# Kernel tuning notes

Hardware: AMD Instinct MI355X
Metric: run time of the kernel (lower is better)

Reference implementation:

```python
import jax, jax.numpy as jnp
import numpy as np

DIM = 4096
N_HEADS = 32
N_KV_HEADS = 8
HEAD_DIM = 128
N_REP = N_HEADS // N_KV_HEADS  # 4
Q_DIM = N_HEADS * HEAD_DIM     # 4096
K_DIM = N_KV_HEADS * HEAD_DIM  # 1024
B, T = 2, 2048
ROPE_THETA = 10000.0


def setup_inputs() -> dict:
    key = jax.random.key(0)
    k1, k2, k3, k4 = jax.random.split(key, 4)
    x = jax.random.normal(k1, (B, T, DIM), dtype=jnp.float32)
    wqkv = jax.random.normal(k2, (Q_DIM + 2 * K_DIM, DIM), dtype=jnp.float32) * 0.02
    wo = jax.random.normal(k3, (DIM, DIM), dtype=jnp.float32) * 0.02
    # RoPE tables: [max_T, head_dim//2]
    inv_freq = 1.0 / (ROPE_THETA ** (jnp.arange(0, HEAD_DIM, 2, dtype=jnp.float32) / HEAD_DIM))
    angles = jnp.arange(T, dtype=jnp.float32)[:, None] * inv_freq[None, :]  # [T, D/2]
    cos = jnp.cos(angles)
    sin = jnp.sin(angles)
    freqs_cis = jax.random.normal(k4, (T, HEAD_DIM // 2), dtype=jnp.float32)  # unused by forward
    return {"x": x, "freqs_cis": freqs_cis, "wqkv": wqkv, "wo": wo, "cos": cos, "sin": sin}


def _apply_rope(q, k, cos, sin):
    # q: [B,T,Hq,D], k: [B,T,Hkv,D]; interleaved even/odd pairs
    Tlen = q.shape[1]
    c = cos[:Tlen][None, :, None, :]  # [1,T,1,D/2]
    s = sin[:Tlen][None, :, None, :]

    def rot(t):
        tr, ti = t[..., 0::2], t[..., 1::2]
        or_ = tr * c - ti * s
        oi = tr * s + ti * c
        return jnp.stack([or_, oi], axis=-1).reshape(t.shape)

    return rot(q), rot(k)


def reference(x, freqs_cis, wqkv, wo, cos, sin):
    Bx, Tx, _ = x.shape
    qkv = jnp.einsum('btd,ed->bte', x, wqkv)  # fused QKV GEMM
    q = qkv[..., :Q_DIM].reshape(Bx, Tx, N_HEADS, HEAD_DIM)
    k = qkv[..., Q_DIM:Q_DIM + K_DIM].reshape(Bx, Tx, N_KV_HEADS, HEAD_DIM)
    v = qkv[..., Q_DIM + K_DIM:].reshape(Bx, Tx, N_KV_HEADS, HEAD_DIM)
    q, k = _apply_rope(q, k, cos, sin)
    # GQA repeat_interleave over head dim
    k = jnp.repeat(k, N_REP, axis=2)  # [B,T,Hq,D]
    v = jnp.repeat(v, N_REP, axis=2)
    scale = 1.0 / jnp.sqrt(jnp.asarray(HEAD_DIM, dtype=q.dtype))
    scores = jnp.einsum('bqhd,bkhd->bhqk', q, k) * scale  # [B,H,T,T]
    causal = jnp.tril(jnp.ones((Tx, Tx), dtype=bool))
    scores = jnp.where(causal[None, None], scores, jnp.finfo(scores.dtype).min)
    probs = jax.nn.softmax(scores, axis=-1)
    y = jnp.einsum('bhqk,bkhd->bqhd', probs, v).reshape(Bx, Tx, Q_DIM)
    return jnp.einsum('btd,ed->bte', y, wo)
```

## Files before the change

kernel.cpp:

```cpp
#include <hip/hip_runtime.h>

#define T_SEQ 2048
#define NB    2
#define NH    32
#define NKV   8
#define HD    128
#define DIM   4096
#define EDIM  6144
#define M_TOK 4096

typedef __bf16          bf8  __attribute__((ext_vector_type(8)));
typedef unsigned short  us8  __attribute__((ext_vector_type(8)));
typedef float           f4   __attribute__((ext_vector_type(4)));
typedef float           f16v __attribute__((ext_vector_type(16)));
typedef int             i4   __attribute__((ext_vector_type(4)));

__device__ inline unsigned short f2bf(float f) {
  unsigned int u = __builtin_bit_cast(unsigned int, f);
  u += 0x7FFF + ((u >> 16) & 1);
  return (unsigned short)(u >> 16);
}
__device__ inline float bf2f(unsigned short h) {
  unsigned int u = ((unsigned int)h) << 16;
  return __builtin_bit_cast(float, u);
}
__device__ inline void gl_lds16(const void* g, void* l) {
  __builtin_amdgcn_global_load_lds(
      (const __attribute__((address_space(1))) unsigned int*)g,
      (__attribute__((address_space(3))) unsigned int*)l, 16, 0, 0);
}
__device__ inline f4 mfma16(bf8 a, bf8 b, f4 c) {
  return __builtin_amdgcn_mfma_f32_16x16x32_bf16(a, b, c, 0, 0, 0);
}
__device__ inline f16v mfma32(bf8 a, bf8 b, f16v c) {
  return __builtin_amdgcn_mfma_f32_32x32x16_bf16(a, b, c, 0, 0, 0);
}
__device__ inline unsigned cvtpk(float lo, float hi) {
  unsigned r;
  asm("v_cvt_pk_bf16_f32 %0, %1, %2" : "=v"(r) : "v"(lo), "v"(hi));
  return r;
}

__global__ void k_f2bf3(const float* __restrict__ x, const float* __restrict__ wq,
                        const float* __restrict__ wo,
                        unsigned short* __restrict__ xb, unsigned short* __restrict__ wqb,
                        unsigned short* __restrict__ wob) {
  const long n0 = (long)M_TOK * DIM / 4;
  const long n1 = (long)EDIM * DIM / 4;
  const long n2 = (long)DIM * DIM / 4;
  const long total = n0 + n1 + n2;
  const long stride = (long)gridDim.x * blockDim.x;
  for (long i = (long)blockIdx.x * blockDim.x + threadIdx.x; i < total; i += stride) {
    const float* in; unsigned short* out; long j = i;
    if (j < n0)              { in = x;  out = xb; }
    else if ((j -= n0) < n1) { in = wq; out = wqb; }
    else       { j -= n1;      in = wo; out = wob; }
    f4 v = *(const f4*)(in + j * 4);
    unsigned long long pack =
        (unsigned long long)f2bf(v[0]) |
        ((unsigned long long)f2bf(v[1]) << 16) |
        ((unsigned long long)f2bf(v[2]) << 32) |
        ((unsigned long long)f2bf(v[3]) << 48);
    *(unsigned long long*)(out + j * 4) = pack;
  }
}

__global__ __launch_bounds__(512, 2)
void k_gemm384(const unsigned short* __restrict__ A, const unsigned short* __restrict__ Bm,
               unsigned short* __restrict__ oQ, unsigned short* __restrict__ oK,
               unsigned short* __restrict__ oV) {
  __shared__ unsigned short As[2][8192];
  __shared__ unsigned short Bs[2][3][8192];
  const int n0 = blockIdx.x;
  const int x = n0 & 7, ix = n0 >> 3;
  const int bm = ((x >> 1) << 3) + (ix >> 3);
  const int bn = ((x & 1) << 3) + (ix & 7);
  const int t = threadIdx.x;
  const int lane = t & 63, w = t >> 6;
  const int wr = w >> 2, wc = w & 3;
  const int l15 = lane & 15, lhi = lane >> 4;
  const int KT = DIM >> 6;

  f4 acc[4][6] = {};

  const int tt0 = t * 8;
  auto stA = [&](int buf, int tile) {
    if (tile >= KT) return;
    const unsigned short* gp = A + (size_t)(bm * 128) * DIM + tile * 64;
#pragma unroll
    for (int j = 0; j < 2; ++j) {
      int e = j * 4096 + tt0;
      int rl = e >> 6, cs = (e & 63) ^ ((rl & 7) << 3);
      gl_lds16(gp + (size_t)rl * DIM + cs, &As[buf][e]);
    }
  };
  auto stB = [&](int buf, int bh, int tile) {
    if (tile >= KT) return;
    const unsigned short* gp = Bm + (size_t)(bn * 384 + bh * 128) * DIM + tile * 64;
#pragma unroll
    for (int j = 0; j < 2; ++j) {
      int e = j * 4096 + tt0;
      int rl = e >> 6, cs = (e & 63) ^ ((rl & 7) << 3);
      gl_lds16(gp + (size_t)rl * DIM + cs, &Bs[buf][bh][e]);
    }
  };
  auto rdA = [&](int buf, int mi, int kk) -> bf8 {
    int row = wr * 64 + mi * 16 + l15;
    int col = (lhi * 8 + kk * 32) ^ ((row & 7) << 3);
    return __builtin_bit_cast(bf8, *(const us8*)&As[buf][row * 64 + col]);
  };
  auto rdB = [&](int buf, int bh, int ni, int kk) -> bf8 {
    int row = wc * 32 + ni * 16 + l15;
    int col = (lhi * 8 + kk * 32) ^ ((row & 7) << 3);
    return __builtin_bit_cast(bf8, *(const us8*)&Bs[buf][bh][row * 64 + col]);
  };
  auto bar = [&]() {
    asm volatile("" ::: "memory");
    __builtin_amdgcn_s_barrier();
    asm volatile("" ::: "memory");
  };
  auto lgkm0 = [&]() {
    asm volatile("s_waitcnt lgkmcnt(0)" ::: "memory");
    __builtin_amdgcn_sched_barrier(0);
  };

  stA(0, 0); stB(0, 0, 0); stB(0, 1, 0); stB(0, 2, 0);
  asm volatile("s_waitcnt vmcnt(4)" ::: "memory");
  bar();

  for (int tp = 0; tp < KT; tp += 2) {
#pragma unroll
    for (int sub = 0; sub < 2; ++sub) {
      const int tc = tp + sub, b = sub;
      const bool last = (tc == KT - 1);
      bf8 af[4][2], bfr[2][2];
#pragma unroll
      for (int mi = 0; mi < 4; ++mi)
#pragma unroll
        for (int kk = 0; kk < 2; ++kk) af[mi][kk] = rdA(b, mi, kk);
#pragma unroll
      for (int ni = 0; ni < 2; ++ni)
#pragma unroll
        for (int kk = 0; kk < 2; ++kk) bfr[ni][kk] = rdB(b, 0, ni, kk);
      stA(b ^ 1, tc + 1); stB(b ^ 1, 0, tc + 1);
      lgkm0();
      __builtin_amdgcn_s_setprio(1);
#pragma unroll
      for (int mi = 0; mi < 4; ++mi)
#pragma unroll
        for (int ni = 0; ni < 2; ++ni)
#pragma unroll
          for (int kk = 0; kk < 2; ++kk)
            acc[mi][ni] = mfma16(af[mi][kk], bfr[ni][kk], acc[mi][ni]);
      __builtin_amdgcn_s_setprio(0);
      if (last) { asm volatile("s_waitcnt vmcnt(2)" ::: "memory"); }
      else      { asm volatile("s_waitcnt vmcnt(6)" ::: "memory"); }
      bar();
#pragma unroll
      for (int ni = 0; ni < 2; ++ni)
#pragma unroll
        for (int kk = 0; kk < 2; ++kk) bfr[ni][kk] = rdB(b, 1, ni, kk);
      stB(b ^ 1, 1, tc + 1);
      lgkm0();
      __builtin_amdgcn_s_setprio(1);
#pragma unroll
      for (int mi = 0; mi < 4; ++mi)
#pragma unroll
        for (int ni = 0; ni < 2; ++ni)
#pragma unroll
          for (int kk = 0; kk < 2; ++kk)
            acc[mi][2 + ni] = mfma16(af[mi][kk], bfr[ni][kk], acc[mi][2 + ni]);
      __builtin_amdgcn_s_setprio(0);
      if (last) { asm volatile("s_waitcnt vmcnt(0)" ::: "memory"); }
      else      { asm volatile("s_waitcnt vmcnt(6)" ::: "memory"); }
      bar();
#pragma unroll
      for (int ni = 0; ni < 2; ++ni)
#pragma unroll
        for (int kk = 0; kk < 2; ++kk) bfr[ni][kk] = rdB(b, 2, ni, kk);
      stB(b ^ 1, 2, tc + 1);
      lgkm0();
      __builtin_amdgcn_s_setprio(1);
#pragma unroll
      for (int mi = 0; mi < 4; ++mi)
#pragma unroll
        for (int ni = 0; ni < 2; ++ni)
#pragma unroll
          for (int kk = 0; kk < 2; ++kk)
            acc[mi][4 + ni] = mfma16(af[mi][kk], bfr[ni][kk], acc[mi][4 + ni]);
      __builtin_amdgcn_s_setprio(0);
      if (!last) { asm volatile("s_waitcnt vmcnt(4)" ::: "memory"); }
      bar();
    }
  }

#pragma unroll
  for (int bh = 0; bh < 3; ++bh)
#pragma unroll
    for (int ni = 0; ni < 2; ++ni) {
      const int colb = bn * 384 + bh * 128 + wc * 32 + ni * 16;
      unsigned short* op; int ldo, c0;
      if (colb < 4096)      { op = oQ; ldo = 4096; c0 = colb; }
      else if (colb < 5120) { op = oK; ldo = 1024; c0 = colb - 4096; }
      else                  { op = oV; ldo = 1024; c0 = colb - 5120; }
#pragma unroll
      for (int mi = 0; mi < 4; ++mi)
#pragma unroll
        for (int rr = 0; rr < 4; ++rr) {
          int row = bm * 128 + wr * 64 + mi * 16 + lhi * 4 + rr;
          op[(size_t)row * ldo + c0 + l15] = f2bf(acc[mi][bh * 2 + ni][rr]);
        }
    }
}

#define MFMA_Q(a0, b0, AF, BF)                                        \
  __builtin_amdgcn_s_setprio(1);                                      \
  _Pragma("unroll") for (int mi = 0; mi < 4; ++mi)                    \
  _Pragma("unroll") for (int ni = 0; ni < 2; ++ni)                    \
  _Pragma("unroll") for (int kk = 0; kk < 2; ++kk)                    \
      acc[(a0) + mi][(b0) + ni] =                                     \
          mfma16(AF[mi][kk], BF[ni][kk], acc[(a0) + mi][(b0) + ni]);  \
  __builtin_amdgcn_s_setprio(0);

#define RD_A(buf, mh)                                                 \
  _Pragma("unroll") for (int mi = 0; mi < 4; ++mi)                    \
  _Pragma("unroll") for (int kk = 0; kk < 2; ++kk)                    \
      af[mi][kk] = rdA(buf, mh, mi, kk);

#define RD_B(buf, nh, BF)                                             \
  _Pragma("unroll") for (int ni = 0; ni < 2; ++ni)                    \
  _Pragma("unroll") for (int kk = 0; kk < 2; ++kk)                    \
      BF[ni][kk] = rdB(buf, nh, ni, kk);

__global__ __launch_bounds__(512, 2)
void k_gemm256f(const unsigned short* __restrict__ A, const unsigned short* __restrict__ Bm,
                float* __restrict__ oF) {
  __shared__ unsigned short As[2][16384];
  __shared__ unsigned short Bs[2][16384];
  const int n0 = blockIdx.x;
  const int x = n0 & 7, ix = n0 >> 3;
  const int bm = ((x >> 1) << 2) + (ix >> 3);
  const int bn = ((x & 1) << 3) + (ix & 7);
  const int N = DIM, K = DIM;
  const int t = threadIdx.x;
  const int lane = t & 63, w = t >> 6;
  const int wr = w >> 2, wc = w & 3;
  const int l15 = lane & 15, lhi = lane >> 4;
  const int KT = K >> 6;
  const int NI = KT >> 1;

  f4 acc[8][4] = {};

  const int tt0 = t * 8;
  auto stA = [&](int buf, int half, int tile) {
    if (tile >= KT) return;
    const unsigned short* gp = A + (size_t)(bm * 256 + half * 128) * K + tile * 64;
#pragma unroll
    for (int j = 0; j < 2; ++j) {
      int e = j * 4096 + tt0;
      int rl = e >> 6;
      int cs = (e & 63) ^ ((rl & 7) << 3);
      gl_lds16(gp + (size_t)rl * K + cs, &As[buf][half * 8192 + e]);
    }
  };
  auto stB = [&](int buf, int half, int tile) {
    if (tile >= KT) return;
    const unsigned short* gp = Bm + (size_t)(bn * 256 + half * 128) * K + tile * 64;
#pragma unroll
    for (int j = 0; j < 2; ++j) {
      int e = j * 4096 + tt0;
      int rl = e >> 6;
      int cs = (e & 63) ^ ((rl & 7) << 3);
      gl_lds16(gp + (size_t)rl * K + cs, &Bs[buf][half * 8192 + e]);
    }
  };
  auto rdA = [&](int buf, int mh, int mi, int kk) -> bf8 {
    int row = mh * 128 + wr * 64 + mi * 16 + l15;
    int col = (lhi * 8 + kk * 32) ^ ((row & 7) << 3);
    return __builtin_bit_cast(bf8, *(const us8*)&As[buf][row * 64 + col]);
  };
  auto rdB = [&](int buf, int nh, int ni, int kk) -> bf8 {
    int row = nh * 128 + wc * 32 + ni * 16 + l15;
    int col = (lhi * 8 + kk * 32) ^ ((row & 7) << 3);
    return __builtin_bit_cast(bf8, *(const us8*)&Bs[buf][row * 64 + col]);
  };
  auto bar = [&]() {
    asm volatile("" ::: "memory");
    __builtin_amdgcn_s_barrier();
    asm volatile("" ::: "memory");
  };
  auto lgkm0 = [&]() {
    asm volatile("s_waitcnt lgkmcnt(0)" ::: "memory");
    __builtin_amdgcn_sched_barrier(0);
  };

  stA(0, 0, 0); stB(0, 1, 0); stA(0, 1, 0); stB(0, 0, 0);
  stA(1, 0, 1); stB(1, 1, 1); stA(1, 1, 1);
  asm volatile("s_waitcnt vmcnt(6)" ::: "memory");
  bar();

  for (int i = 0; i < NI; ++i) {
    const int t2 = 2 * i + 2, t3 = 2 * i + 3;
    bf8 af[4][2], bf0[2][2], bf1[2][2];
    RD_A(0, 0); RD_B(0, 0, bf0);
    stB(1, 0, 2 * i + 1);
    lgkm0();
    MFMA_Q(0, 0, af, bf0);
    bar();
    RD_B(0, 1, bf1);
    stA(0, 0, t2);
    lgkm0();
    MFMA_Q(0, 2, af, bf1);
    bar();
    RD_A(0, 1);
    stB(0, 1, t2);
    lgkm0();
    MFMA_Q(4, 2, af, bf1);
    bar();
    stA(0, 1, t2);
    MFMA_Q(4, 0, af, bf0);
    if (i + 1 < NI) { asm volatile("s_waitcnt vmcnt(6)" ::: "memory"); }
    else            { asm volatile("s_waitcnt vmcnt(0)" ::: "memory"); }
    bar();
    RD_A(1, 0); RD_B(1, 0, bf0);
    stB(0, 0, t2);
    lgkm0();
    MFMA_Q(0, 0, af, bf0);
    bar();
    RD_B(1, 1, bf1);
    stA(1, 0, t3);
    lgkm0();
    MFMA_Q(0, 2, af, bf1);
    bar();
    RD_A(1, 1);
    stB(1, 1, t3);
    lgkm0();
    MFMA_Q(4, 2, af, bf1);
    bar();
    stA(1, 1, t3);
    MFMA_Q(4, 0, af, bf0);
    if (i + 1 < NI) { asm volatile("s_waitcnt vmcnt(6)" ::: "memory"); }
    bar();
  }

  const int rb0 = bm * 256 + wr * 64 + lhi * 4;
  const int cb0 = bn * 256 + wc * 32 + l15;
#pragma unroll
  for (int ai = 0; ai < 8; ++ai)
#pragma unroll
    for (int bj = 0; bj < 4; ++bj)
#pragma unroll
      for (int rr = 0; rr < 4; ++rr) {
        int row = rb0 + (ai >> 2) * 128 + (ai & 3) * 16 + rr;
        int col = cb0 + (bj >> 1) * 128 + (bj & 1) * 16;
        oF[(size_t)row * N + col] = acc[ai][bj][rr];
      }
}

__global__ __launch_bounds__(512, 2)
void k_attn(const unsigned short* __restrict__ Qb, const unsigned short* __restrict__ Kb,
            const unsigned short* __restrict__ Vb, unsigned short* __restrict__ Yb,
            const float* __restrict__ cosp, const float* __restrict__ sinp) {
  __shared__ unsigned short Ks[64 * 128];
  __shared__ unsigned short Vt[128 * 64];
  const int idx = blockIdx.x;
  const int qblk = 7 - (idx >> 6);
  const int h = (idx & 63) >> 1;
  const int b = idx & 1;
  const int kvh = h >> 2;
  const int t = threadIdx.x;
  const int lane = t & 63, w = t >> 6;
  const int l31 = lane & 31, hh = lane >> 5;
  const int qb0 = qblk * 256;
  const int NT = (qblk + 1) * 4;
  const int wqmin = qb0 + w * 32;
  const int q_g = wqmin + l31;
  const float BNEG = -1.0e30f;
  const float QSCALE = (float)(0.08838834764831845 * 1.4426950408889634);

  bf8 qf[8];
  {
    const unsigned short* qp = Qb + (size_t)(b * T_SEQ + q_g) * 4096 + h * 128 + hh * 8;
#pragma unroll
    for (int st = 0; st < 8; ++st) {
      us8 v = *(const us8*)(qp + st * 16);
      f4 c = *(const f4*)(cosp + q_g * 64 + st * 8 + hh * 4);
      f4 s = *(const f4*)(sinp + q_g * 64 + st * 8 + hh * 4);
      us8 o;
#pragma unroll
      for (int j = 0; j < 4; ++j) {
        float tr = bf2f(v[2 * j]), ti = bf2f(v[2 * j + 1]);
        o[2 * j]     = f2bf((tr * c[j] - ti * s[j]) * QSCALE);
        o[2 * j + 1] = f2bf((tr * s[j] + ti * c[j]) * QSCALE);
      }
      qf[st] = __builtin_bit_cast(bf8, o);
    }
  }
  const int swz = (l31 & 7) << 3;
  float m_run = BNEG, l_run = 0.f;
  f16v yacc[4] = {};

  const int krow = t >> 4;
  const int kcol = (t & 15) * 8;
  for (int kt = 0; kt < NT; ++kt) {
    const int kbase = kt * 64;
    const unsigned short* vp = Vb + (size_t)(b * T_SEQ + kbase + lane) * 1024 + kvh * 128 + w * 8;
    us8 vv0 = *(const us8*)vp;
    us8 vv1 = *(const us8*)(vp + 64);
    const unsigned short* kp = Kb + (size_t)(b * T_SEQ + kbase + krow) * 1024 + kvh * 128 + kcol;
    us8 kk0 = *(const us8*)kp;
    us8 kk1 = *(const us8*)(kp + (size_t)32 * 1024);
    f4 kc0 = *(const f4*)(cosp + (kbase + krow) * 64 + (kcol >> 1));
    f4 ks0 = *(const f4*)(sinp + (kbase + krow) * 64 + (kcol >> 1));
    f4 kc1 = *(const f4*)(cosp + (kbase + krow + 32) * 64 + (kcol >> 1));
    f4 ks1 = *(const f4*)(sinp + (kbase + krow + 32) * 64 + (kcol >> 1));
    __syncthreads();
    {
      us8 o0, o1;
#pragma unroll
      for (int j = 0; j < 4; ++j) {
        float tr0 = bf2f(kk0[2 * j]), ti0 = bf2f(kk0[2 * j + 1]);
        o0[2 * j]     = f2bf(tr0 * kc0[j] - ti0 * ks0[j]);
        o0[2 * j + 1] = f2bf(tr0 * ks0[j] + ti0 * kc0[j]);
        float tr1 = bf2f(kk1[2 * j]), ti1 = bf2f(kk1[2 * j + 1]);
        o1[2 * j]     = f2bf(tr1 * kc1[j] - ti1 * ks1[j]);
        o1[2 * j + 1] = f2bf(tr1 * ks1[j] + ti1 * kc1[j]);
      }
      *(us8*)&Ks[krow * 128 + (kcol ^ ((krow & 7) << 3))] = o0;
      *(us8*)&Ks[(krow + 32) * 128 + (kcol ^ ((krow & 7) << 3))] = o1;
    }
#pragma unroll
    for (int j = 0; j < 8; ++j) {
      int d0 = w * 8 + j;
      Vt[(d0 * 64 + lane) ^ ((d0 & 7) << 3)] = vv0[j];
      int d1 = d0 + 64;
      Vt[(d1 * 64 + lane) ^ ((d1 & 7) << 3)] = vv1[j];
    }
    __syncthreads();
    if (kbase > wqmin + 31) continue;

    f16v s0 = {}, s1 = {};
#pragma unroll
    for (int st = 0; st < 8; ++st) {
      int coff = st * 16 + hh * 8;
      bf8 a0 = __builtin_bit_cast(bf8, *(const us8*)&Ks[(l31 * 128 + coff) ^ swz]);
      bf8 a1 = __builtin_bit_cast(bf8, *(const us8*)&Ks[((l31 + 32) * 128 + coff) ^ swz]);
      s0 = mfma32(a0, qf[st], s0);
      s1 = mfma32(a1, qf[st], s1);
    }
    if (kbase + 63 > wqmin) {
#pragma unroll
      for (int r = 0; r < 16; ++r) {
        int kv = kbase + (r & 3) + 8 * (r >> 2) + 4 * hh;
        if (kv > q_g)      s0[r] = BNEG;
        if (kv + 32 > q_g) s1[r] = BNEG;
      }
    }
    float tmax = BNEG;
#pragma unroll
    for (int r = 0; r < 16; ++r) {
      tmax = fmaxf(tmax, s0[r]);
      tmax = fmaxf(tmax, s1[r]);
    }
    tmax = fmaxf(tmax, __shfl_xor(tmax, 32));
    float m_new = fmaxf(m_run, tmax);
    float fac = exp2f(m_run - m_new);
    m_run = m_new;
    float psum = 0.f;
#pragma unroll
    for (int r = 0; r < 16; ++r) {
      s0[r] = exp2f(s0[r] - m_new); psum += s0[r];
      s1[r] = exp2f(s1[r] - m_new); psum += s1[r];
    }
    psum += __shfl_xor(psum, 32);
    l_run = l_run * fac + psum;
    if (!__all(fac == 1.0f)) {
      float facr[16];
#pragma unroll
      for (int r = 0; r < 16; ++r)
        facr[r] = __shfl(fac, (r & 3) + 8 * (r >> 2) + 4 * hh);
#pragma unroll
      for (int dc = 0; dc < 4; ++dc)
#pragma unroll
        for (int r = 0; r < 16; ++r) yacc[dc][r] *= facr[r];
    }
#pragma unroll
    for (int st = 0; st < 4; ++st) {
      f16v sv = (st & 2) ? s1 : s0;
      const int rb = (st & 1) * 8;
      unsigned pkA = cvtpk(sv[rb + 0], sv[rb + 1]);
      unsigned pkB = cvtpk(sv[rb + 2], sv[rb + 3]);
      unsigned pkC = cvtpk(sv[rb + 4], sv[rb + 5]);
      unsigned pkD = cvtpk(sv[rb + 6], sv[rb + 7]);
      unsigned xA = __shfl_xor(pkA, 32);
      unsigned xB = __shfl_xor(pkB, 32);
      unsigned xC = __shfl_xor(pkC, 32);
      unsigned xD = __shfl_xor(pkD, 32);
      unsigned w0 = hh ? xC : pkA;
      unsigned w1 = hh ? xD : pkB;
      unsigned w2 = hh ? pkC : xA;
      unsigned w3 = hh ? pkD : xB;
      i4 wi = { (int)w0, (int)w1, (int)w2, (int)w3 };
      bf8 pf = __builtin_bit_cast(bf8, wi);
#pragma unroll
      for (int dc = 0; dc < 4; ++dc) {
        int d = dc * 32 + l31;
        bf8 vf = __builtin_bit_cast(bf8, *(const us8*)&Vt[(d * 64 + st * 16 + hh * 8) ^ swz]);
        yacc[dc] = mfma32(pf, vf, yacc[dc]);
      }
    }
  }
  float inv_l = 1.0f / l_run;
  float il[16];
#pragma unroll
  for (int r = 0; r < 16; ++r)
    il[r] = __shfl(inv_l, (r & 3) + 8 * (r >> 2) + 4 * hh);
#pragma unroll
  for (int dc = 0; dc < 4; ++dc)
#pragma unroll
    for (int r = 0; r < 16; ++r) {
      int qrow = qb0 + w * 32 + (r & 3) + 8 * (r >> 2) + 4 * hh;
      Yb[(size_t)(b * T_SEQ + qrow) * 4096 + h * 128 + dc * 32 + l31] =
          f2bf(yacc[dc][r] * il[r]);
    }
}

extern "C" void kernel_launch(void* const* d_in, const int* in_sizes, int n_in,
                              void* d_out, int out_size, void* d_ws, size_t ws_size,
                              hipStream_t stream) {
  const float* x    = (const float*)d_in[0];
  const float* wqkv = (const float*)d_in[2];
  const float* wo   = (const float*)d_in[3];
  const float* cosp = (const float*)d_in[4];
  const float* sinp = (const float*)d_in[5];
  float* out = (float*)d_out;

  char* ws = (char*)d_ws;
  size_t o = 0;
  auto alloc = [&](size_t bytes) { void* p = ws + o; o += (bytes + 255) & ~(size_t)255; return p; };
  unsigned short* x_b    = (unsigned short*)alloc((size_t)M_TOK * DIM * 2);
  unsigned short* wqkv_b = (unsigned short*)alloc((size_t)EDIM * DIM * 2);
  unsigned short* wo_b   = (unsigned short*)alloc((size_t)DIM * DIM * 2);
  unsigned short* Qb     = (unsigned short*)alloc((size_t)M_TOK * 4096 * 2);
  unsigned short* Kb     = (unsigned short*)alloc((size_t)M_TOK * 1024 * 2);
  unsigned short* Vb     = (unsigned short*)alloc((size_t)M_TOK * 1024 * 2);
  unsigned short* Yb     = (unsigned short*)alloc((size_t)M_TOK * 4096 * 2);
  if (o > ws_size) return;

  k_f2bf3<<<2048, 256, 0, stream>>>(x, wqkv, wo, x_b, wqkv_b, wo_b);

  k_gemm384<<<dim3(512), 512, 0, stream>>>(x_b, wqkv_b, Qb, Kb, Vb);

  k_attn<<<dim3(512, 1, 1), 512, 0, stream>>>(Qb, Kb, Vb, Yb, cosp, sinp);

  k_gemm256f<<<dim3(256), 512, 0, stream>>>(Yb, wo_b, out);
}
```

Before: 513.3 us.

## Software-pipeline LDS fragment reads across QKV GEMM sub-stages

Restructures the QKV GEMM main loop so LDS reads of the next stage's A and B0 fragments, and of the B1/B2 fragments, are issued ahead of the MFMA blocks that need them. Partial lgkmcnt waits replace full drains, so LDS latency can overlap with MFMA execution. The vmcnt and barrier placement is reworked to match the new load ordering. In exchange it holds more fragments in registers (double-buffered A and B0), which raises VGPR pressure, and the tuned wait counts are fragile.

```diff
diff --git a/kernel.cpp b/kernel.cpp
--- a/kernel.cpp
+++ b/kernel.cpp
@@ -119,67 +119,52 @@
     __builtin_amdgcn_s_barrier();
     asm volatile("" ::: "memory");
   };
-  auto lgkm0 = [&]() {
-    asm volatile("s_waitcnt lgkmcnt(0)" ::: "memory");
-    __builtin_amdgcn_sched_barrier(0);
-  };
 
   stA(0, 0); stB(0, 0, 0); stB(0, 1, 0); stB(0, 2, 0);
-  asm volatile("s_waitcnt vmcnt(4)" ::: "memory");
+  asm volatile("s_waitcnt vmcnt(2)" ::: "memory");
   bar();
 
+  bf8 af[2][4][2], b0f[2][2][2], bfA[2][2], bfB[2][2];
+#pragma unroll
+  for (int mi = 0; mi < 4; ++mi)
+#pragma unroll
+    for (int kk = 0; kk < 2; ++kk) af[0][mi][kk] = rdA(0, mi, kk);
+#pragma unroll
+  for (int ni = 0; ni < 2; ++ni)
+#pragma unroll
+    for (int kk = 0; kk < 2; ++kk) b0f[0][ni][kk] = rdB(0, 0, ni, kk);
+
   for (int tp = 0; tp < KT; tp += 2) {
 #pragma unroll
     for (int sub = 0; sub < 2; ++sub) {
-      const int tc = tp + sub, b = sub;
+      const int tc = tp + sub, p = sub;
       const bool last = (tc == KT - 1);
-      bf8 af[4][2], bfr[2][2];
+      stA(p ^ 1, tc + 1); stB(p ^ 1, 0, tc + 1);
+#pragma unroll
+      for (int ni = 0; ni < 2; ++ni)
+#pragma unroll
+        for (int kk = 0; kk < 2; ++kk) bfA[ni][kk] = rdB(p, 1, ni, kk);
+      asm volatile("s_waitcnt lgkmcnt(4)" ::: "memory");
+      __builtin_amdgcn_sched_barrier(0);
+      __builtin_amdgcn_s_setprio(1);
 #pragma unroll
       for (int mi = 0; mi < 4; ++mi)
 #pragma unroll
-        for (int kk = 0; kk < 2; ++kk) af[mi][kk] = rdA(b, mi, kk);
-#pragma unroll
-      for (int ni = 0; ni < 2; ++ni)
-#pragma unroll
-        for (int kk = 0; kk < 2; ++kk) bfr[ni][kk] = rdB(b, 0, ni, kk);
-      stA(b ^ 1, tc + 1); stB(b ^ 1, 0, tc + 1);
-      lgkm0();
-      __builtin_amdgcn_s_setprio(1);
-#pragma unroll
-      for (int mi = 0; mi < 4; ++mi)
-#pragma unroll
         for (int ni = 0; ni < 2; ++ni)
 #pragma unroll
           for (int kk = 0; kk < 2; ++kk)
-            acc[mi][ni] = mfma16(af[mi][kk], bfr[ni][kk], acc[mi][ni]);
-      __builtin_amdgcn_s_setprio(0);
-      if (last) { asm volatile("s_waitcnt vmcnt(2)" ::: "memory"); }
-      else      { asm volatile("s_waitcnt vmcnt(6)" ::: "memory"); }
-      bar();
-#pragma unroll
-      for (int ni = 0; ni < 2; ++ni)
-#pragma unroll
-        for (int kk = 0; kk < 2; ++kk) bfr[ni][kk] = rdB(b, 1, ni, kk);
-      stB(b ^ 1, 1, tc + 1);
-      lgkm0();
-      __builtin_amdgcn_s_setprio(1);
-#pragma unroll
-      for (int mi = 0; mi < 4; ++mi)
-#pragma unroll
-        for (int ni = 0; ni < 2; ++ni)
-#pragma unroll
-          for (int kk = 0; kk < 2; ++kk)
-            acc[mi][2 + ni] = mfma16(af[mi][kk], bfr[ni][kk], acc[mi][2 + ni]);
+            acc[mi][ni] = mfma16(af[p][mi][kk], b0f[p][ni][kk], acc[mi][ni]);
       __builtin_amdgcn_s_setprio(0);
       if (last) { asm volatile("s_waitcnt vmcnt(0)" ::: "memory"); }
-      else      { asm volatile("s_waitcnt vmcnt(6)" ::: "memory"); }
+      else      { asm volatile("s_waitcnt vmcnt(4)" ::: "memory"); }
       bar();
+      stB(p ^ 1, 1, tc + 1);
 #pragma unroll
       for (int ni = 0; ni < 2; ++ni)
 #pragma unroll
-        for (int kk = 0; kk < 2; ++kk) bfr[ni][kk] = rdB(b, 2, ni, kk);
-      stB(b ^ 1, 2, tc + 1);
-      lgkm0();
+        for (int kk = 0; kk < 2; ++kk) bfB[ni][kk] = rdB(p, 2, ni, kk);
+      asm volatile("s_waitcnt lgkmcnt(4)" ::: "memory");
+      __builtin_amdgcn_sched_barrier(0);
       __builtin_amdgcn_s_setprio(1);
 #pragma unroll
       for (int mi = 0; mi < 4; ++mi)
@@ -187,10 +172,39 @@
         for (int ni = 0; ni < 2; ++ni)
 #pragma unroll
           for (int kk = 0; kk < 2; ++kk)
-            acc[mi][4 + ni] = mfma16(af[mi][kk], bfr[ni][kk], acc[mi][4 + ni]);
+            acc[mi][2 + ni] = mfma16(af[p][mi][kk], bfA[ni][kk], acc[mi][2 + ni]);
       __builtin_amdgcn_s_setprio(0);
-      if (!last) { asm volatile("s_waitcnt vmcnt(4)" ::: "memory"); }
+      if (last) { asm volatile("s_waitcnt vmcnt(0)" ::: "memory"); }
+      else      { asm volatile("s_waitcnt vmcnt(2)" ::: "memory"); }
       bar();
+      stB(p ^ 1, 2, tc + 1);
+      if (!last) {
+#pragma unroll
+        for (int mi = 0; mi < 4; ++mi)
+#pragma unroll
+          for (int kk = 0; kk < 2; ++kk) af[p ^ 1][mi][kk] = rdA(p ^ 1, mi, kk);
+#pragma unroll
+        for (int ni = 0; ni < 2; ++ni)
+#pragma unroll
+          for (int kk = 0; kk < 2; ++kk) b0f[p ^ 1][ni][kk] = rdB(p ^ 1, 0, ni, kk);
+        asm volatile("s_waitcnt lgkmcnt(12)" ::: "memory");
+      } else {
+        asm volatile("s_waitcnt lgkmcnt(0)" ::: "memory");
+      }
+      __builtin_amdgcn_sched_barrier(0);
+      __builtin_amdgcn_s_setprio(1);
+#pragma unroll
+      for (int mi = 0; mi < 4; ++mi)
+#pragma unroll
+        for (int ni = 0; ni < 2; ++ni)
+#pragma unroll
+          for (int kk = 0; kk < 2; ++kk)
+            acc[mi][4 + ni] = mfma16(af[p][mi][kk], bfB[ni][kk], acc[mi][4 + ni]);
+      __builtin_amdgcn_s_setprio(0);
+      if (!last) {
+        asm volatile("s_waitcnt vmcnt(2)" ::: "memory");
+        bar();
+      }
     }
   }
 
```

Measured after the change: 598.0 us. 16.5% more time.
